# Performance work log

Hardware: AMD Instinct MI355X
Metric: run time of the kernel (lower is better)

## Reference

```python
import jax, jax.numpy as jnp
import numpy as np

B, P = 8, 1024
D = 512
BUCKETS = 65536
LS = (8, 7, 6)  # padded ids per patch for ngrams 1,2,3


def setup_inputs() -> dict:
    key = jax.random.key(0)
    ks = jax.random.split(key, 10)
    inp = {}
    for i, L in enumerate(LS):
        inp[f"ids_{i+1}"] = jax.random.randint(ks[i], (B, P, L), 0, BUCKETS, dtype=jnp.int64)
        inp[f"mask_{i+1}"] = jax.random.randint(ks[3 + i], (B, P, L), 0, 2, dtype=jnp.int32).astype(bool)
        inp[f"emb_{i+1}"] = jax.random.normal(ks[6 + i], (BUCKETS, D), dtype=jnp.float32)
    inp["patch_mask"] = jax.random.randint(ks[9], (B, P), 0, 2, dtype=jnp.int32).astype(bool)
    return inp


def reference(ids_1, ids_2, ids_3, mask_1, mask_2, mask_3, patch_mask, emb_1, emb_2, emb_3):
    # For each ngram order: gather [B,P,L,D], zero out padded ids, sum over L.
    out = jnp.zeros((B, P, D), dtype=emb_1.dtype)
    for ids, m, emb in ((ids_1, mask_1, emb_1), (ids_2, mask_2, emb_2), (ids_3, mask_3, emb_3)):
        g = jnp.take(emb, ids, axis=0)               # [B,P,L,D]
        out = out + jnp.where(m[..., None], g, 0).sum(axis=2)
    return jnp.where(patch_mask[..., None], out, 0)
```

## Files before the change

### kernel.cpp

```cpp
#include <hip/hip_runtime.h>


#define D_DIM 512
#define NPATCH 8192

__device__ __forceinline__ void acc_add(float4& a, const float4 b) {
    a.x += b.x; a.y += b.y; a.z += b.z; a.w += b.w;
}

template <int L>
__device__ __forceinline__ void gather_sum(const int* __restrict__ ids,
                                           const int* __restrict__ mask,
                                           const float* __restrict__ emb,
                                           int lane, float4& acc0, float4& acc1) {
#pragma unroll
    for (int l = 0; l < L; ++l) {
        if (mask[l]) {
            const float4* row = (const float4*)(emb + (size_t)ids[l] * D_DIM);
            acc_add(acc0, row[lane]);
            acc_add(acc1, row[64 + lane]);
        }
    }
}

__global__ __launch_bounds__(256) void patch_embed_kernel(
    const int* __restrict__ ids1, const int* __restrict__ m1, const float* __restrict__ e1,
    const int* __restrict__ ids2, const int* __restrict__ m2, const float* __restrict__ e2,
    const int* __restrict__ ids3, const int* __restrict__ m3, const float* __restrict__ e3,
    const int* __restrict__ pmask, float* __restrict__ out) {
    const int wave  = threadIdx.x >> 6;
    const int lane  = threadIdx.x & 63;
    const int patch = (blockIdx.x << 2) | wave;

    float4 acc0 = make_float4(0.f, 0.f, 0.f, 0.f);
    float4 acc1 = make_float4(0.f, 0.f, 0.f, 0.f);

    if (pmask[patch]) {
        gather_sum<8>(ids1 + patch * 8, m1 + patch * 8, e1, lane, acc0, acc1);
        gather_sum<7>(ids2 + patch * 7, m2 + patch * 7, e2, lane, acc0, acc1);
        gather_sum<6>(ids3 + patch * 6, m3 + patch * 6, e3, lane, acc0, acc1);
    }

    float4* outv = (float4*)(out + (size_t)patch * D_DIM);
    outv[lane]      = acc0;
    outv[64 + lane] = acc1;
}

extern "C" void kernel_launch(void* const* d_in, const int* in_sizes, int n_in,
                              void* d_out, int out_size, void* d_ws, size_t ws_size,
                              hipStream_t stream) {
    const int*   ids1  = (const int*)d_in[0];
    const int*   m1    = (const int*)d_in[1];
    const float* e1    = (const float*)d_in[2];
    const int*   ids2  = (const int*)d_in[3];
    const int*   m2    = (const int*)d_in[4];
    const float* e2    = (const float*)d_in[5];
    const int*   ids3  = (const int*)d_in[6];
    const int*   m3    = (const int*)d_in[7];
    const float* e3    = (const float*)d_in[8];
    const int*   pmask = (const int*)d_in[9];
    float* out = (float*)d_out;

    dim3 grid(NPATCH / 4);
    dim3 block(256);
    patch_embed_kernel<<<grid, block, 0, stream>>>(ids1, m1, e1, ids2, m2, e2,
                                                   ids3, m3, e3, pmask, out);
}
```

Baseline: 310.3 us.

## Split each patch across two waves and issue all row loads branch-free

Each patch is now handled by two waves, each covering half of the 512-wide row, which doubles the grid. Ids and masks are read once per wave through readfirstlane. All 21 gather loads are issued up front without branches: masked rows point at row 0 and are multiplied by a zero weight. The aim is more memory-level parallelism and fewer divergent branches, so more loads are in flight at once. The cost is loading row 0 for every masked-out id, which adds traffic, and higher register pressure from holding 21 float4 results.

Result: no change. 310.5 us (+0.0%).

```diff
diff --git a/kernel.cpp b/kernel.cpp
--- a/kernel.cpp
+++ b/kernel.cpp
@@ -3,47 +3,61 @@
 
 #define D_DIM 512
 #define NPATCH 8192
-
-__device__ __forceinline__ void acc_add(float4& a, const float4 b) {
-    a.x += b.x; a.y += b.y; a.z += b.z; a.w += b.w;
-}
-
-template <int L>
-__device__ __forceinline__ void gather_sum(const int* __restrict__ ids,
-                                           const int* __restrict__ mask,
-                                           const float* __restrict__ emb,
-                                           int lane, float4& acc0, float4& acc1) {
-#pragma unroll
-    for (int l = 0; l < L; ++l) {
-        if (mask[l]) {
-            const float4* row = (const float4*)(emb + (size_t)ids[l] * D_DIM);
-            acc_add(acc0, row[lane]);
-            acc_add(acc1, row[64 + lane]);
-        }
-    }
-}
+#define NGATHER 21
 
 __global__ __launch_bounds__(256) void patch_embed_kernel(
     const int* __restrict__ ids1, const int* __restrict__ m1, const float* __restrict__ e1,
     const int* __restrict__ ids2, const int* __restrict__ m2, const float* __restrict__ e2,
     const int* __restrict__ ids3, const int* __restrict__ m3, const float* __restrict__ e3,
     const int* __restrict__ pmask, float* __restrict__ out) {
-    const int wave  = threadIdx.x >> 6;
-    const int lane  = threadIdx.x & 63;
-    const int patch = (blockIdx.x << 2) | wave;
+    const int tid   = threadIdx.x;
+    const int wave  = tid >> 6;
+    const int lane  = tid & 63;
+    const int gwave = (blockIdx.x << 2) | wave;
+    const int patch = gwave >> 1;
+    const int fidx  = ((gwave & 1) << 6) | lane;
 
-    float4 acc0 = make_float4(0.f, 0.f, 0.f, 0.f);
-    float4 acc1 = make_float4(0.f, 0.f, 0.f, 0.f);
+    float4 acc = make_float4(0.f, 0.f, 0.f, 0.f);
 
     if (pmask[patch]) {
-        gather_sum<8>(ids1 + patch * 8, m1 + patch * 8, e1, lane, acc0, acc1);
-        gather_sum<7>(ids2 + patch * 7, m2 + patch * 7, e2, lane, acc0, acc1);
-        gather_sum<6>(ids3 + patch * 6, m3 + patch * 6, e3, lane, acc0, acc1);
+        const float* base[NGATHER];
+        float        w[NGATHER];
+
+        const int* idp[3]  = {ids1 + patch * 8, ids2 + patch * 7, ids3 + patch * 6};
+        const int* mp[3]   = {m1 + patch * 8,   m2 + patch * 7,   m3 + patch * 6};
+        const float* ep[3] = {e1, e2, e3};
+        const int  Ln[3]   = {8, 7, 6};
+
+        int k = 0;
+#pragma unroll
+        for (int n = 0; n < 3; ++n) {
+#pragma unroll
+            for (int l = 0; l < 8; ++l) {
+                if (l < Ln[n]) {
+                    const int id = __builtin_amdgcn_readfirstlane(idp[n][l]);
+                    const int m  = __builtin_amdgcn_readfirstlane(mp[n][l]);
+                    base[k] = ep[n] + (size_t)(m ? id : 0) * D_DIM;
+                    w[k]    = m ? 1.0f : 0.0f;
+                    ++k;
+                }
+            }
+        }
+
+        float4 r[NGATHER];
+#pragma unroll
+        for (int i = 0; i < NGATHER; ++i)
+            r[i] = ((const float4*)base[i])[fidx];
+
+#pragma unroll
+        for (int i = 0; i < NGATHER; ++i) {
+            acc.x += w[i] * r[i].x;
+            acc.y += w[i] * r[i].y;
+            acc.z += w[i] * r[i].z;
+            acc.w += w[i] * r[i].w;
+        }
     }
 
-    float4* outv = (float4*)(out + (size_t)patch * D_DIM);
-    outv[lane]      = acc0;
-    outv[64 + lane] = acc1;
+    ((float4*)(out + (size_t)patch * D_DIM))[fidx] = acc;
 }
 
 extern "C" void kernel_launch(void* const* d_in, const int* in_sizes, int n_in,
@@ -61,7 +75,7 @@
     const int*   pmask = (const int*)d_in[9];
     float* out = (float*)d_out;
 
-    dim3 grid(NPATCH / 4);
+    dim3 grid(NPATCH * 2 / 4);
     dim3 block(256);
     patch_embed_kernel<<<grid, block, 0, stream>>>(ids1, m1, e1, ids2, m2, e2,
                                                    ids3, m3, e3, pmask, out);
```
